# Performance work log

Hardware: AMD Instinct MI355X
Metric: run time of the kernel (lower is better)

## Reference

```python
import jax, jax.numpy as jnp
import numpy as np

DIM = 768


def setup_inputs() -> dict:
    key = jax.random.key(0)
    k1, k2, k3, k4, k5 = jax.random.split(key, 5)
    lines = jax.random.normal(k1, (32, 512, DIM), dtype=jnp.float32)
    videos = jax.random.normal(k2, (32, 128, DIM), dtype=jnp.float32)
    video_mask = jax.random.randint(k3, (32, 128), 0, 2, dtype=jnp.int32)
    # nn.Linear(dim, dim, bias=False) weights, applied as x @ W.T
    w_q = jax.random.normal(k4, (DIM, DIM), dtype=jnp.float32) * (DIM ** -0.5)
    w_k = jax.random.normal(k5, (DIM, DIM), dtype=jnp.float32) * (DIM ** -0.5)
    return {"lines": lines, "videos": videos, "video_mask": video_mask, "w_q": w_q, "w_k": w_k}


def reference(lines, videos, video_mask, w_q, w_k):
    scale = DIM ** -0.5
    q = jnp.einsum('bld,ed->ble', lines, w_q)   # (B, L, D)
    k = jnp.einsum('bvd,ed->bve', videos, w_k)  # (B, V, D)
    scores = jnp.einsum('bld,bvd->blv', q, k) * scale
    pad = (video_mask == 0)[:, None, :]          # (B, 1, V)
    scores = jnp.where(pad, jnp.float32(-1e9), scores)
    weights = jax.nn.softmax(scores, axis=-1)    # (B, L, V)
    return jnp.einsum('blv,bvd->bld', weights, videos)
```

## Files before the change

kernel.cpp:

```cpp
#include <hip/hip_runtime.h>

#define DIM 768
#define NB  32
#define LQ  512
#define NV  128

typedef unsigned short u16;
typedef unsigned int   u32;
typedef __bf16 bf16x8 __attribute__((ext_vector_type(8)));
typedef float  f32x4  __attribute__((ext_vector_type(4)));
typedef u16    u16x8  __attribute__((ext_vector_type(8)));
typedef u16    u16x4  __attribute__((ext_vector_type(4)));

typedef __attribute__((address_space(1))) const void gvoid;
typedef __attribute__((address_space(3))) void       svoid;

__device__ __forceinline__ u16 f2bf(float f) {
    u32 u = __float_as_uint(f);
    return (u16)((u + 0x7FFFu + ((u >> 16) & 1u)) >> 16);
}

__device__ __forceinline__ bf16x8 ld_frag(const u16* p) {
    return __builtin_bit_cast(bf16x8, *(const u16x8*)p);
}

__device__ __forceinline__ void gld16(const void* g, void* l) {
    __builtin_amdgcn_global_load_lds((gvoid*)g, (svoid*)l, 16, 0, 0);
}

#define W2S    4
#define W2_BLK (36 * W2S)

__global__ __launch_bounds__(256) void prep_kernel(const float* __restrict__ w_q,
                                                   const float* __restrict__ w_k,
                                                   const float* __restrict__ videos,
                                                   float* __restrict__ w2f,
                                                   u16* __restrict__ vt2,
                                                   u16* __restrict__ vbf) {
    __shared__ union {
        u16 T[64][136];
        struct { u16 q[128][72]; u16 k[128][72]; } w2s;
    } uL;
    const int bx = blockIdx.x;
    const int t  = threadIdx.x;

    if (bx < W2_BLK) {
        const int tile = bx / W2S, kc = bx % W2S;
        const int m0 = (tile / 6) * 128;
        const int n0 = (tile % 6) * 128;
        const int w    = t >> 6;
        const int lane = t & 63;
        const int quad = lane >> 4;
        const int ln   = lane & 15;
        const int wr   = (w >> 1) * 64;
        const int wc   = (w & 1) * 64;
        f32x4 acc[4][4] = {};
        for (int ks = kc * 3; ks < kc * 3 + 3; ++ks) {
            __syncthreads();
            const int e0 = ks * 64;
#pragma unroll
            for (int p = 0; p < 8; ++p) {
                int f  = t + p * 256;
                int r  = f >> 5;
                int c4 = f & 31;
                float4 xq = *(const float4*)(w_q + (size_t)(e0 + r) * DIM + m0 + c4 * 4);
                float4 xk = *(const float4*)(w_k + (size_t)(e0 + r) * DIM + n0 + c4 * 4);
                int swz = ((r >> 3) ^ ((c4 >> 1) & 7)) * 8 + (r & 7);
                uL.w2s.q[c4 * 4 + 0][swz] = f2bf(xq.x);
                uL.w2s.q[c4 * 4 + 1][swz] = f2bf(xq.y);
                uL.w2s.q[c4 * 4 + 2][swz] = f2bf(xq.z);
                uL.w2s.q[c4 * 4 + 3][swz] = f2bf(xq.w);
                uL.w2s.k[c4 * 4 + 0][swz] = f2bf(xk.x);
                uL.w2s.k[c4 * 4 + 1][swz] = f2bf(xk.y);
                uL.w2s.k[c4 * 4 + 2][swz] = f2bf(xk.z);
                uL.w2s.k[c4 * 4 + 3][swz] = f2bf(xk.w);
            }
            __syncthreads();
#pragma unroll
            for (int kk = 0; kk < 2; ++kk) {
                bf16x8 af[4], bfr[4];
#pragma unroll
                for (int i = 0; i < 4; ++i) {
                    int row = wr + i * 16 + ln;
                    af[i]  = ld_frag(&uL.w2s.q[row][((kk * 4 + quad) ^ ((row >> 3) & 7)) * 8]);
                }
#pragma unroll
                for (int j = 0; j < 4; ++j) {
                    int row = wc + j * 16 + ln;
                    bfr[j] = ld_frag(&uL.w2s.k[row][((kk * 4 + quad) ^ ((row >> 3) & 7)) * 8]);
                }
#pragma unroll
                for (int i = 0; i < 4; ++i)
#pragma unroll
                    for (int j = 0; j < 4; ++j)
                        acc[i][j] = __builtin_amdgcn_mfma_f32_16x16x32_bf16(af[i], bfr[j], acc[i][j], 0, 0, 0);
            }
        }
#pragma unroll
        for (int i = 0; i < 4; ++i)
#pragma unroll
            for (int j = 0; j < 4; ++j)
#pragma unroll
                for (int r = 0; r < 4; ++r)
                    atomicAdd(&w2f[(size_t)(m0 + wr + i * 16 + quad * 4 + r) * DIM +
                                   n0 + wc + j * 16 + ln], acc[i][j][r]);
        return;
    }

    const int v  = bx - W2_BLK;
    const int b  = v / 12;
    const int d0 = (v % 12) * 64;
    const float* src = videos + (size_t)b * NV * DIM;
#pragma unroll
    for (int p = 0; p < 8; ++p) {
        int f  = t + p * 256;
        int vv = f >> 4;
        int c4 = f & 15;
        float4 x = *(const float4*)(src + (size_t)vv * DIM + d0 + c4 * 4);
        u16x4 o = { f2bf(x.x), f2bf(x.y), f2bf(x.z), f2bf(x.w) };
        uL.T[c4 * 4 + 0][vv] = o[0];
        uL.T[c4 * 4 + 1][vv] = o[1];
        uL.T[c4 * 4 + 2][vv] = o[2];
        uL.T[c4 * 4 + 3][vv] = o[3];
        *(u16x4*)(vbf + ((size_t)b * NV + vv) * DIM + d0 + c4 * 4) = o;
    }
    __syncthreads();
#pragma unroll
    for (int p = 0; p < 4; ++p) {
        int f  = t + p * 256;
        int dl = f >> 4;
        int v8 = f & 15;
        int d  = d0 + dl;
        int it = d >> 7, wv = (d >> 4) & 7, lnn = d & 15;
        int ks = v8 >> 2, qd = v8 & 3;
        int lane = qd * 16 + lnn;
        size_t off = ((((size_t)b * 6 + it) * 8 + wv) * 4 + ks) * 512 + lane * 8;
        *(u16x8*)(vt2 + off) = *(const u16x8*)&uL.T[dl][v8 * 8];
    }
}

__global__ __launch_bounds__(512) void g_kernel(const u16* __restrict__ A,
                                                const float* __restrict__ Wf,
                                                u16* __restrict__ C) {
    __shared__ u16 sA[128][64];
    __shared__ u16 sB[128][72];
    const int t    = threadIdx.x;
    const int w    = t >> 6;
    const int lane = t & 63;
    const int quad = lane >> 4;
    const int ln   = lane & 15;

    int m0, n0;
    {
        int i = blockIdx.x;
        int xcd = i & 7, s = i >> 3;
        m0 = ((s / 6) * 8 + xcd) * 128;
        n0 = (s % 6) * 128;
    }

    const int wr = (w >> 2) * 64;
    const int wc = (w & 3) * 32;
    const int srow   = lane >> 3;
    const int schunk = (lane & 7) ^ srow;

    f32x4 acc[4][2] = {};
#pragma unroll
    for (int ks = 0; ks < 12; ++ks) {
        __syncthreads();
#pragma unroll
        for (int p = 0; p < 2; ++p) {
            int rb = w * 16 + p * 8;
            gld16(A + (size_t)(m0 + rb + srow) * DIM + ks * 64 + schunk * 8, &sA[rb][0]);
        }
#pragma unroll
        for (int p = 0; p < 4; ++p) {
            int idx = t + p * 512;
            int row = idx >> 4, c4 = idx & 15;
            float4 x = *(const float4*)(Wf + (size_t)(n0 + row) * DIM + ks * 64 + c4 * 4);
            u16x4 o = { f2bf(x.x), f2bf(x.y), f2bf(x.z), f2bf(x.w) };
            int swz = ((c4 >> 1) ^ (row & 7)) * 8 + (c4 & 1) * 4;
            *(u16x4*)&sB[row][swz] = o;
        }
        __syncthreads();
#pragma unroll
        for (int kk = 0; kk < 2; ++kk) {
            bf16x8 af[4], bfr[2];
#pragma unroll
            for (int i = 0; i < 4; ++i)
                af[i]  = ld_frag(&sA[wr + i * 16 + ln][((kk * 4 + quad) ^ (ln & 7)) * 8]);
#pragma unroll
            for (int j = 0; j < 2; ++j)
                bfr[j] = ld_frag(&sB[wc + j * 16 + ln][((kk * 4 + quad) ^ (ln & 7)) * 8]);
#pragma unroll
            for (int i = 0; i < 4; ++i)
#pragma unroll
                for (int j = 0; j < 2; ++j)
                    acc[i][j] = __builtin_amdgcn_mfma_f32_16x16x32_bf16(af[i], bfr[j], acc[i][j], 0, 0, 0);
        }
    }
#pragma unroll
    for (int i = 0; i < 4; ++i)
#pragma unroll
        for (int j = 0; j < 2; ++j)
#pragma unroll
            for (int r = 0; r < 4; ++r)
                C[(size_t)(m0 + wr + i * 16 + quad * 4 + r) * DIM + n0 + wc + j * 16 + ln] =
                    f2bf(acc[i][j][r]);
}

__global__ __launch_bounds__(512) void attn_kernel(const float* __restrict__ Qf,
                                                   const u16* __restrict__ K,
                                                   const u16* __restrict__ Vt2,
                                                   const int* __restrict__ mask,
                                                   float* __restrict__ out) {
    int b, l0;
    {
        int i = blockIdx.x;
        int xcd = i & 7, s = i >> 3;
        b  = (s >> 3) * 8 + xcd;
        l0 = (s & 7) * 64;
    }
    const int t    = threadIdx.x;
    const int w    = t >> 6;
    const int lane = t & 63;
    const int quad = lane >> 4;
    const int ln   = lane & 15;

    __shared__ union {
        struct { u16 q[2][64][64]; u16 k[2][128][64]; } st;
        float s[64][132];
    } uA;
    __shared__ u16 sP[64][136];
    __shared__ float sBias[128];

    const float* Qb = Qf + ((size_t)b * LQ + l0) * DIM;
    const u16*   Kb = K + (size_t)b * NV * DIM;
    if (t < NV) sBias[t] = mask[b * NV + t] ? 0.0f : -1e9f;

    const int srow   = lane >> 3;
    const int schunk = (lane & 7) ^ srow;
    const int qrow = t >> 3;
    const int qc8  = t & 7;
    const int qswz = (qc8 ^ (qrow & 7)) * 8;

    auto stageK = [&](int ks, int sel) {
        gld16(Kb + (size_t)(w * 16 + srow) * DIM + ks * 64 + schunk * 8, &uA.st.k[sel][w * 16][0]);
        gld16(Kb + (size_t)(w * 16 + 8 + srow) * DIM + ks * 64 + schunk * 8, &uA.st.k[sel][w * 16 + 8][0]);
    };
    auto loadQ = [&](int ks, float4& x0, float4& x1) {
        const float* p = Qb + (size_t)qrow * DIM + ks * 64 + qc8 * 8;
        x0 = *(const float4*)p;
        x1 = *(const float4*)(p + 4);
    };
    auto writeQ = [&](int sel, const float4& x0, const float4& x1) {
        u16x8 o = { f2bf(x0.x), f2bf(x0.y), f2bf(x0.z), f2bf(x0.w),
                    f2bf(x1.x), f2bf(x1.y), f2bf(x1.z), f2bf(x1.w) };
        *(u16x8*)&uA.st.q[sel][qrow][qswz] = o;
    };

    f32x4 accS[4] = {};
    {
        float4 x0, x1;
        loadQ(0, x0, x1);
        stageK(0, 0);
        writeQ(0, x0, x1);
    }
#pragma unroll
    for (int ks = 0; ks < 12; ++ks) {
        __syncthreads();
        const int sel = ks & 1;
        float4 nx0, nx1;
        if (ks < 11) {
            loadQ(ks + 1, nx0, nx1);
            stageK(ks + 1, sel ^ 1);
        }
#pragma unroll
        for (int kk = 0; kk < 2; ++kk) {
            bf16x8 bfr = ld_frag(&uA.st.k[sel][w * 16 + ln][((kk * 4 + quad) ^ (ln & 7)) * 8]);
#pragma unroll
            for (int i = 0; i < 4; ++i) {
                bf16x8 af = ld_frag(&uA.st.q[sel][i * 16 + ln][((kk * 4 + quad) ^ (ln & 7)) * 8]);
                accS[i] = __builtin_amdgcn_mfma_f32_16x16x32_bf16(af, bfr, accS[i], 0, 0, 0);
            }
        }
        if (ks < 11) writeQ(sel ^ 1, nx0, nx1);
    }
    __syncthreads();
    const float scale = 0.03608439182435161f;
#pragma unroll
    for (int i = 0; i < 4; ++i)
#pragma unroll
        for (int r = 0; r < 4; ++r)
            uA.s[i * 16 + quad * 4 + r][w * 16 + ln] = accS[i][r] * scale;
    __syncthreads();

    {
        const int row = t >> 3, seg = t & 7;
        float vals[16];
        float mx = -3.0e38f;
#pragma unroll
        for (int c = 0; c < 4; ++c) {
            float4 x  = *(const float4*)&uA.s[row][seg * 16 + c * 4];
            float4 bz = *(const float4*)&sBias[seg * 16 + c * 4];
            float a0 = x.x + bz.x, a1 = x.y + bz.y, a2 = x.z + bz.z, a3 = x.w + bz.w;
            vals[c * 4 + 0] = a0; vals[c * 4 + 1] = a1;
            vals[c * 4 + 2] = a2; vals[c * 4 + 3] = a3;
            mx = fmaxf(mx, fmaxf(fmaxf(a0, a1), fmaxf(a2, a3)));
        }
        mx = fmaxf(mx, __shfl_xor(mx, 1));
        mx = fmaxf(mx, __shfl_xor(mx, 2));
        mx = fmaxf(mx, __shfl_xor(mx, 4));
        float sum = 0.0f;
#pragma unroll
        for (int c = 0; c < 16; ++c) { float e = __expf(vals[c] - mx); vals[c] = e; sum += e; }
        sum += __shfl_xor(sum, 1);
        sum += __shfl_xor(sum, 2);
        sum += __shfl_xor(sum, 4);
        const float inv = 1.0f / sum;
#pragma unroll
        for (int h = 0; h < 2; ++h) {
            u16x8 pk;
#pragma unroll
            for (int e = 0; e < 8; ++e) pk[e] = f2bf(vals[h * 8 + e] * inv);
            *(u16x8*)&sP[row][seg * 16 + h * 8] = pk;
        }
    }
    __syncthreads();

    bf16x8 paf[4][4];
#pragma unroll
    for (int i = 0; i < 4; ++i)
#pragma unroll
        for (int ks = 0; ks < 4; ++ks)
            paf[i][ks] = ld_frag(&sP[i * 16 + ln][ks * 32 + quad * 8]);

    const u16* V2 = Vt2 + (size_t)b * 6 * 8 * 4 * 512;
    float*     Ob = out + ((size_t)b * LQ + l0) * DIM;
    for (int it = 0; it < 6; ++it) {
        f32x4 accO[4] = {};
#pragma unroll
        for (int ks = 0; ks < 4; ++ks) {
            bf16x8 bv = ld_frag(V2 + (((size_t)(it * 8 + w)) * 4 + ks) * 512 + lane * 8);
#pragma unroll
            for (int i = 0; i < 4; ++i)
                accO[i] = __builtin_amdgcn_mfma_f32_16x16x32_bf16(paf[i][ks], bv, accO[i], 0, 0, 0);
        }
#pragma unroll
        for (int i = 0; i < 4; ++i)
#pragma unroll
            for (int r = 0; r < 4; ++r)
                Ob[(size_t)(i * 16 + quad * 4 + r) * DIM + it * 128 + w * 16 + ln] = accO[i][r];
    }
}

extern "C" void kernel_launch(void* const* d_in, const int* in_sizes, int n_in,
                              void* d_out, int out_size, void* d_ws, size_t ws_size,
                              hipStream_t stream) {
    const float* lines  = (const float*)d_in[0];
    const float* videos = (const float*)d_in[1];
    const int*   mask   = (const int*)d_in[2];
    const float* w_q    = (const float*)d_in[3];
    const float* w_k    = (const float*)d_in[4];
    float*       out    = (float*)d_out;

    u16*   gw  = (u16*)d_ws;
    u16*   vt2 = gw  + (size_t)NB * NV * DIM;
    u16*   vbf = vt2 + (size_t)NB * DIM * NV;
    float* w2f = (float*)(vbf + (size_t)NB * NV * DIM);

    hipMemsetAsync(w2f, 0, (size_t)DIM * DIM * sizeof(float), stream);
    prep_kernel<<<W2_BLK + 384, 256, 0, stream>>>(w_q, w_k, videos, w2f, vt2, vbf);
    g_kernel   <<<192, 512, 0, stream>>>(vbf, w2f, gw);
    attn_kernel<<<256, 512, 0, stream>>>(lines, gw, vt2, mask, out);
}
```

Baseline: 165.5 us.

## Fuse prep, G and attention kernels into one cooperative persistent kernel

Replaces the memset plus three kernel launches with a single cooperative kernel of 256 blocks. Grid-wide syncs separate the phases: weight-product and video conversion, then the video-weight GEMM, then attention. The weight-product phase now covers the full K range in 36 blocks and writes the result directly, so the split-K atomics and the memset go away. This removes launch gaps and tail effects between kernels. In exchange, phase 1 uses only 36 blocks for the weight product, and the grid syncs and shared-memory union may limit occupancy. The old multi-kernel path is kept as a fallback if the cooperative launch fails.

```diff
diff --git a/kernel.cpp b/kernel.cpp
--- a/kernel.cpp
+++ b/kernel.cpp
@@ -1,4 +1,7 @@
 #include <hip/hip_runtime.h>
+#include <hip/hip_cooperative_groups.h>
+
+namespace cg = cooperative_groups;
 
 #define DIM 768
 #define NB  32
@@ -26,6 +29,321 @@
 
 __device__ __forceinline__ void gld16(const void* g, void* l) {
     __builtin_amdgcn_global_load_lds((gvoid*)g, (svoid*)l, 16, 0, 0);
+}
+
+__global__ __launch_bounds__(512) void fused_kernel(const float* __restrict__ lines,
+                                                    const float* __restrict__ videos,
+                                                    const int*   __restrict__ mask,
+                                                    const float* __restrict__ w_q,
+                                                    const float* __restrict__ w_k,
+                                                    float* __restrict__ out,
+                                                    u16* __restrict__ gw,
+                                                    u16* __restrict__ vt2,
+                                                    u16* __restrict__ vbf,
+                                                    float* __restrict__ w2f) {
+    __shared__ union {
+        struct { u16 q[128][72]; u16 k[128][72]; } w2s;
+        u16 T[2][64][136];
+        struct { u16 A[128][64]; u16 B[128][72]; } gs;
+        struct {
+            union {
+                struct { u16 q[2][64][64]; u16 k[2][128][64]; } st;
+                float s[64][132];
+            } u;
+            u16 p[64][136];
+            float bias[128];
+        } at;
+    } sm;
+
+    const int bx   = blockIdx.x;
+    const int t    = threadIdx.x;
+    const int w    = t >> 6;
+    const int lane = t & 63;
+    const int quad = lane >> 4;
+    const int ln   = lane & 15;
+
+    if (bx < 36) {
+        const int m0 = (bx / 6) * 128;
+        const int n0 = (bx % 6) * 128;
+        const int wr = (w >> 1) * 32;
+        const int wc = (w & 1) * 64;
+        f32x4 acc[2][4] = {};
+        for (int ks = 0; ks < 12; ++ks) {
+            __syncthreads();
+            const int e0 = ks * 64;
+#pragma unroll
+            for (int p = 0; p < 4; ++p) {
+                int f  = t + p * 512;
+                int r  = f >> 5;
+                int c4 = f & 31;
+                float4 xq = *(const float4*)(w_q + (size_t)(e0 + r) * DIM + m0 + c4 * 4);
+                float4 xk = *(const float4*)(w_k + (size_t)(e0 + r) * DIM + n0 + c4 * 4);
+                int swz = ((r >> 3) ^ ((c4 >> 1) & 7)) * 8 + (r & 7);
+                sm.w2s.q[c4 * 4 + 0][swz] = f2bf(xq.x);
+                sm.w2s.q[c4 * 4 + 1][swz] = f2bf(xq.y);
+                sm.w2s.q[c4 * 4 + 2][swz] = f2bf(xq.z);
+                sm.w2s.q[c4 * 4 + 3][swz] = f2bf(xq.w);
+                sm.w2s.k[c4 * 4 + 0][swz] = f2bf(xk.x);
+                sm.w2s.k[c4 * 4 + 1][swz] = f2bf(xk.y);
+                sm.w2s.k[c4 * 4 + 2][swz] = f2bf(xk.z);
+                sm.w2s.k[c4 * 4 + 3][swz] = f2bf(xk.w);
+            }
+            __syncthreads();
+#pragma unroll
+            for (int kk = 0; kk < 2; ++kk) {
+                bf16x8 af[2], bfr[4];
+#pragma unroll
+                for (int i = 0; i < 2; ++i) {
+                    int row = wr + i * 16 + ln;
+                    af[i]  = ld_frag(&sm.w2s.q[row][((kk * 4 + quad) ^ ((row >> 3) & 7)) * 8]);
+                }
+#pragma unroll
+                for (int j = 0; j < 4; ++j) {
+                    int row = wc + j * 16 + ln;
+                    bfr[j] = ld_frag(&sm.w2s.k[row][((kk * 4 + quad) ^ ((row >> 3) & 7)) * 8]);
+                }
+#pragma unroll
+                for (int i = 0; i < 2; ++i)
+#pragma unroll
+                    for (int j = 0; j < 4; ++j)
+                        acc[i][j] = __builtin_amdgcn_mfma_f32_16x16x32_bf16(af[i], bfr[j], acc[i][j], 0, 0, 0);
+            }
+        }
+#pragma unroll
+        for (int i = 0; i < 2; ++i)
+#pragma unroll
+            for (int j = 0; j < 4; ++j)
+#pragma unroll
+                for (int r = 0; r < 4; ++r)
+                    w2f[(size_t)(m0 + wr + i * 16 + quad * 4 + r) * DIM +
+                        n0 + wc + j * 16 + ln] = acc[i][j][r];
+    } else if (bx < 36 + 192) {
+        const int unit0 = (bx - 36) * 2;
+        if (unit0 < 384) {
+            const int half = t >> 8;
+            const int tl   = t & 255;
+            const int v    = unit0 + half;
+            const int b    = v / 12;
+            const int d0   = (v % 12) * 64;
+            const float* src = videos + (size_t)b * NV * DIM;
+#pragma unroll
+            for (int p = 0; p < 8; ++p) {
+                int f  = tl + p * 256;
+                int vv = f >> 4;
+                int c4 = f & 15;
+                float4 x = *(const float4*)(src + (size_t)vv * DIM + d0 + c4 * 4);
+                u16x4 o = { f2bf(x.x), f2bf(x.y), f2bf(x.z), f2bf(x.w) };
+                sm.T[half][c4 * 4 + 0][vv] = o[0];
+                sm.T[half][c4 * 4 + 1][vv] = o[1];
+                sm.T[half][c4 * 4 + 2][vv] = o[2];
+                sm.T[half][c4 * 4 + 3][vv] = o[3];
+                *(u16x4*)(vbf + ((size_t)b * NV + vv) * DIM + d0 + c4 * 4) = o;
+            }
+            __syncthreads();
+#pragma unroll
+            for (int p = 0; p < 4; ++p) {
+                int f  = tl + p * 256;
+                int dl = f >> 4;
+                int v8 = f & 15;
+                int d  = d0 + dl;
+                int it = d >> 7, wv = (d >> 4) & 7, lnn = d & 15;
+                int ksv = v8 >> 2, qd = v8 & 3;
+                int lane2 = qd * 16 + lnn;
+                size_t off = ((((size_t)b * 6 + it) * 8 + wv) * 4 + ksv) * 512 + lane2 * 8;
+                *(u16x8*)(vt2 + off) = *(const u16x8*)&sm.T[half][dl][v8 * 8];
+            }
+        }
+    }
+
+    cg::this_grid().sync();
+
+    if (bx < 192) {
+        int m0, n0;
+        {
+            int i = bx;
+            int xcd = i & 7, s = i >> 3;
+            m0 = ((s / 6) * 8 + xcd) * 128;
+            n0 = (s % 6) * 128;
+        }
+        const int wr = (w >> 2) * 64;
+        const int wc = (w & 3) * 32;
+        const int srow   = lane >> 3;
+        const int schunk = (lane & 7) ^ srow;
+
+        f32x4 acc[4][2] = {};
+#pragma unroll
+        for (int ks = 0; ks < 12; ++ks) {
+            __syncthreads();
+#pragma unroll
+            for (int p = 0; p < 2; ++p) {
+                int rb = w * 16 + p * 8;
+                gld16(vbf + (size_t)(m0 + rb + srow) * DIM + ks * 64 + schunk * 8, &sm.gs.A[rb][0]);
+            }
+#pragma unroll
+            for (int p = 0; p < 4; ++p) {
+                int idx = t + p * 512;
+                int row = idx >> 4, c4 = idx & 15;
+                float4 x = *(const float4*)(w2f + (size_t)(n0 + row) * DIM + ks * 64 + c4 * 4);
+                u16x4 o = { f2bf(x.x), f2bf(x.y), f2bf(x.z), f2bf(x.w) };
+                int swz = ((c4 >> 1) ^ (row & 7)) * 8 + (c4 & 1) * 4;
+                *(u16x4*)&sm.gs.B[row][swz] = o;
+            }
+            __syncthreads();
+#pragma unroll
+            for (int kk = 0; kk < 2; ++kk) {
+                bf16x8 af[4], bfr[2];
+#pragma unroll
+                for (int i = 0; i < 4; ++i)
+                    af[i]  = ld_frag(&sm.gs.A[wr + i * 16 + ln][((kk * 4 + quad) ^ (ln & 7)) * 8]);
+#pragma unroll
+                for (int j = 0; j < 2; ++j)
+                    bfr[j] = ld_frag(&sm.gs.B[wc + j * 16 + ln][((kk * 4 + quad) ^ (ln & 7)) * 8]);
+#pragma unroll
+                for (int i = 0; i < 4; ++i)
+#pragma unroll
+                    for (int j = 0; j < 2; ++j)
+                        acc[i][j] = __builtin_amdgcn_mfma_f32_16x16x32_bf16(af[i], bfr[j], acc[i][j], 0, 0, 0);
+            }
+        }
+#pragma unroll
+        for (int i = 0; i < 4; ++i)
+#pragma unroll
+            for (int j = 0; j < 2; ++j)
+#pragma unroll
+                for (int r = 0; r < 4; ++r)
+                    gw[(size_t)(m0 + wr + i * 16 + quad * 4 + r) * DIM + n0 + wc + j * 16 + ln] =
+                        f2bf(acc[i][j][r]);
+    }
+
+    cg::this_grid().sync();
+
+    {
+        int b, l0;
+        {
+            int i = bx;
+            int xcd = i & 7, s = i >> 3;
+            b  = (s >> 3) * 8 + xcd;
+            l0 = (s & 7) * 64;
+        }
+        const float* Qb = lines + ((size_t)b * LQ + l0) * DIM;
+        const u16*   Kb = gw + (size_t)b * NV * DIM;
+        if (t < NV) sm.at.bias[t] = mask[b * NV + t] ? 0.0f : -1e9f;
+
+        const int srow   = lane >> 3;
+        const int schunk = (lane & 7) ^ srow;
+        const int qrow = t >> 3;
+        const int qc8  = t & 7;
+        const int qswz = (qc8 ^ (qrow & 7)) * 8;
+
+        auto stageK = [&](int ks, int sel) {
+            gld16(Kb + (size_t)(w * 16 + srow) * DIM + ks * 64 + schunk * 8, &sm.at.u.st.k[sel][w * 16][0]);
+            gld16(Kb + (size_t)(w * 16 + 8 + srow) * DIM + ks * 64 + schunk * 8, &sm.at.u.st.k[sel][w * 16 + 8][0]);
+        };
+        auto loadQ = [&](int ks, float4& x0, float4& x1) {
+            const float* p = Qb + (size_t)qrow * DIM + ks * 64 + qc8 * 8;
+            x0 = *(const float4*)p;
+            x1 = *(const float4*)(p + 4);
+        };
+        auto writeQ = [&](int sel, const float4& x0, const float4& x1) {
+            u16x8 o = { f2bf(x0.x), f2bf(x0.y), f2bf(x0.z), f2bf(x0.w),
+                        f2bf(x1.x), f2bf(x1.y), f2bf(x1.z), f2bf(x1.w) };
+            *(u16x8*)&sm.at.u.st.q[sel][qrow][qswz] = o;
+        };
+
+        f32x4 accS[4] = {};
+        {
+            float4 x0, x1;
+            loadQ(0, x0, x1);
+            stageK(0, 0);
+            writeQ(0, x0, x1);
+        }
+#pragma unroll
+        for (int ks = 0; ks < 12; ++ks) {
+            __syncthreads();
+            const int sel = ks & 1;
+            float4 nx0, nx1;
+            if (ks < 11) {
+                loadQ(ks + 1, nx0, nx1);
+                stageK(ks + 1, sel ^ 1);
+            }
+#pragma unroll
+            for (int kk = 0; kk < 2; ++kk) {
+                bf16x8 bfr = ld_frag(&sm.at.u.st.k[sel][w * 16 + ln][((kk * 4 + quad) ^ (ln & 7)) * 8]);
+#pragma unroll
+                for (int i = 0; i < 4; ++i) {
+                    bf16x8 af = ld_frag(&sm.at.u.st.q[sel][i * 16 + ln][((kk * 4 + quad) ^ (ln & 7)) * 8]);
+                    accS[i] = __builtin_amdgcn_mfma_f32_16x16x32_bf16(af, bfr, accS[i], 0, 0, 0);
+                }
+            }
+            if (ks < 11) writeQ(sel ^ 1, nx0, nx1);
+        }
+        __syncthreads();
+        const float scale = 0.03608439182435161f;
+#pragma unroll
+        for (int i = 0; i < 4; ++i)
+#pragma unroll
+            for (int r = 0; r < 4; ++r)
+                sm.at.u.s[i * 16 + quad * 4 + r][w * 16 + ln] = accS[i][r] * scale;
+        __syncthreads();
+
+        {
+            const int row = t >> 3, seg = t & 7;
+            float vals[16];
+            float mx = -3.0e38f;
+#pragma unroll
+            for (int c = 0; c < 4; ++c) {
+                float4 x  = *(const float4*)&sm.at.u.s[row][seg * 16 + c * 4];
+                float4 bz = *(const float4*)&sm.at.bias[seg * 16 + c * 4];
+                float a0 = x.x + bz.x, a1 = x.y + bz.y, a2 = x.z + bz.z, a3 = x.w + bz.w;
+                vals[c * 4 + 0] = a0; vals[c * 4 + 1] = a1;
+                vals[c * 4 + 2] = a2; vals[c * 4 + 3] = a3;
+                mx = fmaxf(mx, fmaxf(fmaxf(a0, a1), fmaxf(a2, a3)));
+            }
+            mx = fmaxf(mx, __shfl_xor(mx, 1));
+            mx = fmaxf(mx, __shfl_xor(mx, 2));
+            mx = fmaxf(mx, __shfl_xor(mx, 4));
+            float sum = 0.0f;
+#pragma unroll
+            for (int c = 0; c < 16; ++c) { float e = __expf(vals[c] - mx); vals[c] = e; sum += e; }
+            sum += __shfl_xor(sum, 1);
+            sum += __shfl_xor(sum, 2);
+            sum += __shfl_xor(sum, 4);
+            const float inv = 1.0f / sum;
+#pragma unroll
+            for (int h = 0; h < 2; ++h) {
+                u16x8 pk;
+#pragma unroll
+                for (int e = 0; e < 8; ++e) pk[e] = f2bf(vals[h * 8 + e] * inv);
+                *(u16x8*)&sm.at.p[row][seg * 16 + h * 8] = pk;
+            }
+        }
+        __syncthreads();
+
+        bf16x8 paf[4][4];
+#pragma unroll
+        for (int i = 0; i < 4; ++i)
+#pragma unroll
+            for (int ks = 0; ks < 4; ++ks)
+                paf[i][ks] = ld_frag(&sm.at.p[i * 16 + ln][ks * 32 + quad * 8]);
+
+        const u16* V2 = vt2 + (size_t)b * 6 * 8 * 4 * 512;
+        float*     Ob = out + ((size_t)b * LQ + l0) * DIM;
+        for (int it = 0; it < 6; ++it) {
+            f32x4 accO[4] = {};
+#pragma unroll
+            for (int ks = 0; ks < 4; ++ks) {
+                bf16x8 bv = ld_frag(V2 + (((size_t)(it * 8 + w)) * 4 + ks) * 512 + lane * 8);
+#pragma unroll
+                for (int i = 0; i < 4; ++i)
+                    accO[i] = __builtin_amdgcn_mfma_f32_16x16x32_bf16(paf[i][ks], bv, accO[i], 0, 0, 0);
+            }
+#pragma unroll
+            for (int i = 0; i < 4; ++i)
+#pragma unroll
+                for (int r = 0; r < 4; ++r)
+                    Ob[(size_t)(i * 16 + quad * 4 + r) * DIM + it * 128 + w * 16 + ln] = accO[i][r];
+        }
+    }
 }
 
 #define W2S    4
@@ -368,8 +686,15 @@
     u16*   vbf = vt2 + (size_t)NB * DIM * NV;
     float* w2f = (float*)(vbf + (size_t)NB * NV * DIM);
 
-    hipMemsetAsync(w2f, 0, (size_t)DIM * DIM * sizeof(float), stream);
-    prep_kernel<<<W2_BLK + 384, 256, 0, stream>>>(w_q, w_k, videos, w2f, vt2, vbf);
-    g_kernel   <<<192, 512, 0, stream>>>(vbf, w2f, gw);
-    attn_kernel<<<256, 512, 0, stream>>>(lines, gw, vt2, mask, out);
+    void* args[] = { (void*)&lines, (void*)&videos, (void*)&mask, (void*)&w_q,
+                     (void*)&w_k, (void*)&out, (void*)&gw, (void*)&vt2,
+                     (void*)&vbf, (void*)&w2f };
+    hipError_t err = hipLaunchCooperativeKernel((void*)fused_kernel, dim3(256), dim3(512),
+                                                args, 0, stream);
+    if (err != hipSuccess) {
+        hipMemsetAsync(w2f, 0, (size_t)DIM * DIM * sizeof(float), stream);
+        prep_kernel<<<W2_BLK + 384, 256, 0, stream>>>(w_q, w_k, videos, w2f, vt2, vbf);
+        g_kernel   <<<192, 512, 0, stream>>>(vbf, w2f, gw);
+        attn_kernel<<<256, 512, 0, stream>>>(lines, gw, vt2, mask, out);
+    }
 }
```

New measurement: 248.1 us. 49.9% more time.

## Fuse prep, K-projection and attention into one persistent kernel with flag sync

Applied to the files above, without the earlier changes.

Replaces the three kernel launches with a single 256-block kernel. Blocks run prep, then the W2/K GEMM, then attention, and wait on global atomic flags for the inputs each stage needs. The W2 split-K partials now go to four separate buffers that the GEMM sums, instead of using atomicAdd into a zeroed buffer. This removes the launch gaps and kernel-boundary serialization between stages. In exchange it adds spin-waits that assume all 256 blocks are resident at once, a larger union of shared memory, and extra global reads to sum the partials.

```diff
diff --git a/kernel.cpp b/kernel.cpp
--- a/kernel.cpp
+++ b/kernel.cpp
@@ -4,6 +4,7 @@
 #define NB  32
 #define LQ  512
 #define NV  128
+#define W2SZ 589824
 
 typedef unsigned short u16;
 typedef unsigned int   u32;
@@ -28,328 +29,362 @@
     __builtin_amdgcn_global_load_lds((gvoid*)g, (svoid*)l, 16, 0, 0);
 }
 
-#define W2S    4
-#define W2_BLK (36 * W2S)
-
-__global__ __launch_bounds__(256) void prep_kernel(const float* __restrict__ w_q,
-                                                   const float* __restrict__ w_k,
-                                                   const float* __restrict__ videos,
-                                                   float* __restrict__ w2f,
-                                                   u16* __restrict__ vt2,
-                                                   u16* __restrict__ vbf) {
+#define FW2 0
+#define FVB 8
+#define FVT 40
+#define FK  72
+
+__device__ __forceinline__ void wait_ge(int* p, int n) {
+    int iters = 0;
+    while (__hip_atomic_load(p, __ATOMIC_RELAXED, __HIP_MEMORY_SCOPE_AGENT) < n) {
+        __builtin_amdgcn_s_sleep(2);
+        if (++iters > (1 << 20)) break;
+    }
+    (void)__hip_atomic_load(p, __ATOMIC_ACQUIRE, __HIP_MEMORY_SCOPE_AGENT);
+}
+
+__global__ __launch_bounds__(512, 2) void mega_kernel(const float* __restrict__ lines,
+                                                      const float* __restrict__ videos,
+                                                      const int*   __restrict__ mask,
+                                                      const float* __restrict__ w_q,
+                                                      const float* __restrict__ w_k,
+                                                      float* __restrict__ out,
+                                                      u16* __restrict__ gw,
+                                                      u16* __restrict__ vt2,
+                                                      u16* __restrict__ vbf,
+                                                      float* __restrict__ w2f,
+                                                      int* __restrict__ flags) {
     __shared__ union {
-        u16 T[64][136];
         struct { u16 q[128][72]; u16 k[128][72]; } w2s;
-    } uL;
-    const int bx = blockIdx.x;
-    const int t  = threadIdx.x;
-
-    if (bx < W2_BLK) {
-        const int tile = bx / W2S, kc = bx % W2S;
+        u16 T[2][64][136];
+        struct { u16 A[128][64]; u16 B[128][72]; } gs;
+        struct {
+            union {
+                struct { u16 q[2][64][64]; u16 k[2][128][64]; } st;
+                float s[64][132];
+            } u;
+            u16 p[64][136];
+            float bias[128];
+        } at;
+    } sm;
+
+    const int bx   = blockIdx.x;
+    const int t    = threadIdx.x;
+    const int w    = t >> 6;
+    const int lane = t & 63;
+    const int quad = lane >> 4;
+    const int ln   = lane & 15;
+
+    if (bx < 144) {
+        const int tile = bx >> 2, kc = bx & 3;
         const int m0 = (tile / 6) * 128;
         const int n0 = (tile % 6) * 128;
-        const int w    = t >> 6;
-        const int lane = t & 63;
-        const int quad = lane >> 4;
-        const int ln   = lane & 15;
-        const int wr   = (w >> 1) * 64;
-        const int wc   = (w & 1) * 64;
-        f32x4 acc[4][4] = {};
+        const int wr = (w >> 1) * 32;
+        const int wc = (w & 1) * 64;
+        f32x4 acc[2][4] = {};
         for (int ks = kc * 3; ks < kc * 3 + 3; ++ks) {
             __syncthreads();
             const int e0 = ks * 64;
 #pragma unroll
-            for (int p = 0; p < 8; ++p) {
-                int f  = t + p * 256;
+            for (int p = 0; p < 4; ++p) {
+                int f  = t + p * 512;
                 int r  = f >> 5;
                 int c4 = f & 31;
                 float4 xq = *(const float4*)(w_q + (size_t)(e0 + r) * DIM + m0 + c4 * 4);
                 float4 xk = *(const float4*)(w_k + (size_t)(e0 + r) * DIM + n0 + c4 * 4);
                 int swz = ((r >> 3) ^ ((c4 >> 1) & 7)) * 8 + (r & 7);
-                uL.w2s.q[c4 * 4 + 0][swz] = f2bf(xq.x);
-                uL.w2s.q[c4 * 4 + 1][swz] = f2bf(xq.y);
-                uL.w2s.q[c4 * 4 + 2][swz] = f2bf(xq.z);
-                uL.w2s.q[c4 * 4 + 3][swz] = f2bf(xq.w);
-                uL.w2s.k[c4 * 4 + 0][swz] = f2bf(xk.x);
-                uL.w2s.k[c4 * 4 + 1][swz] = f2bf(xk.y);
-                uL.w2s.k[c4 * 4 + 2][swz] = f2bf(xk.z);
-                uL.w2s.k[c4 * 4 + 3][swz] = f2bf(xk.w);
+                sm.w2s.q[c4 * 4 + 0][swz] = f2bf(xq.x);
+                sm.w2s.q[c4 * 4 + 1][swz] = f2bf(xq.y);
+                sm.w2s.q[c4 * 4 + 2][swz] = f2bf(xq.z);
+                sm.w2s.q[c4 * 4 + 3][swz] = f2bf(xq.w);
+                sm.w2s.k[c4 * 4 + 0][swz] = f2bf(xk.x);
+                sm.w2s.k[c4 * 4 + 1][swz] = f2bf(xk.y);
+                sm.w2s.k[c4 * 4 + 2][swz] = f2bf(xk.z);
+                sm.w2s.k[c4 * 4 + 3][swz] = f2bf(xk.w);
             }
             __syncthreads();
 #pragma unroll
             for (int kk = 0; kk < 2; ++kk) {
-                bf16x8 af[4], bfr[4];
-#pragma unroll
-                for (int i = 0; i < 4; ++i) {
+                bf16x8 af[2], bfr[4];
+#pragma unroll
+                for (int i = 0; i < 2; ++i) {
                     int row = wr + i * 16 + ln;
-                    af[i]  = ld_frag(&uL.w2s.q[row][((kk * 4 + quad) ^ ((row >> 3) & 7)) * 8]);
+                    af[i]  = ld_frag(&sm.w2s.q[row][((kk * 4 + quad) ^ ((row >> 3) & 7)) * 8]);
                 }
 #pragma unroll
                 for (int j = 0; j < 4; ++j) {
                     int row = wc + j * 16 + ln;
-                    bfr[j] = ld_frag(&uL.w2s.k[row][((kk * 4 + quad) ^ ((row >> 3) & 7)) * 8]);
+                    bfr[j] = ld_frag(&sm.w2s.k[row][((kk * 4 + quad) ^ ((row >> 3) & 7)) * 8]);
                 }
 #pragma unroll
-                for (int i = 0; i < 4; ++i)
+                for (int i = 0; i < 2; ++i)
 #pragma unroll
                     for (int j = 0; j < 4; ++j)
                         acc[i][j] = __builtin_amdgcn_mfma_f32_16x16x32_bf16(af[i], bfr[j], acc[i][j], 0, 0, 0);
             }
         }
+        float* wp = w2f + (size_t)kc * W2SZ;
+#pragma unroll
+        for (int i = 0; i < 2; ++i)
+#pragma unroll
+            for (int j = 0; j < 4; ++j)
+#pragma unroll
+                for (int r = 0; r < 4; ++r)
+                    wp[(size_t)(m0 + wr + i * 16 + quad * 4 + r) * DIM +
+                       n0 + wc + j * 16 + ln] = acc[i][j][r];
+        __syncthreads();
+        if (t == 0) { __threadfence(); atomicAdd(&flags[FW2 + tile / 6], 1); }
+    } else if (bx < 240) {
+        const int half = t >> 8;
+        const int tl   = t & 255;
+        for (int pass = 0; pass < 2; ++pass) {
+            const int v  = (bx - 144) * 4 + pass * 2 + half;
+            const int b  = v / 12;
+            const int d0 = (v % 12) * 64;
+            const float* src = videos + (size_t)b * NV * DIM;
+            if (pass) __syncthreads();
+#pragma unroll
+            for (int p = 0; p < 8; ++p) {
+                int f  = tl + p * 256;
+                int vv = f >> 4;
+                int c4 = f & 15;
+                float4 x = *(const float4*)(src + (size_t)vv * DIM + d0 + c4 * 4);
+                u16x4 o = { f2bf(x.x), f2bf(x.y), f2bf(x.z), f2bf(x.w) };
+                sm.T[half][c4 * 4 + 0][vv] = o[0];
+                sm.T[half][c4 * 4 + 1][vv] = o[1];
+                sm.T[half][c4 * 4 + 2][vv] = o[2];
+                sm.T[half][c4 * 4 + 3][vv] = o[3];
+                *(u16x4*)(vbf + ((size_t)b * NV + vv) * DIM + d0 + c4 * 4) = o;
+            }
+            __syncthreads();
+#pragma unroll
+            for (int p = 0; p < 4; ++p) {
+                int f  = tl + p * 256;
+                int dl = f >> 4;
+                int v8 = f & 15;
+                int d  = d0 + dl;
+                int it = d >> 7, wv = (d >> 4) & 7, lnn = d & 15;
+                int ksv = v8 >> 2, qd = v8 & 3;
+                int lane2 = qd * 16 + lnn;
+                size_t off = ((((size_t)b * 6 + it) * 8 + wv) * 4 + ksv) * 512 + lane2 * 8;
+                *(u16x8*)(vt2 + off) = *(const u16x8*)&sm.T[half][dl][v8 * 8];
+            }
+            __syncthreads();
+            if (tl == 0) {
+                __threadfence();
+                atomicAdd(&flags[FVB + b], 1);
+                atomicAdd(&flags[FVT + b], 1);
+            }
+        }
+    }
+
+    if (bx < 192) {
+        int m0, n0;
+        {
+            int i = bx;
+            int xcd = i & 7, s = i >> 3;
+            m0 = ((s / 6) * 8 + xcd) * 128;
+            n0 = (s % 6) * 128;
+        }
+        const int gb = m0 >> 7;
+        if (t == 0) {
+            wait_ge(&flags[FW2 + (n0 >> 7)], 24);
+            wait_ge(&flags[FVB + gb], 12);
+        }
+        __syncthreads();
+
+        const int wr = (w >> 2) * 64;
+        const int wc = (w & 3) * 32;
+        const int srow   = lane >> 3;
+        const int schunk = (lane & 7) ^ srow;
+
+        f32x4 acc[4][2] = {};
+#pragma unroll
+        for (int ks = 0; ks < 12; ++ks) {
+            __syncthreads();
+#pragma unroll
+            for (int p = 0; p < 2; ++p) {
+                int rb = w * 16 + p * 8;
+                gld16(vbf + (size_t)(m0 + rb + srow) * DIM + ks * 64 + schunk * 8, &sm.gs.A[rb][0]);
+            }
+#pragma unroll
+            for (int p = 0; p < 4; ++p) {
+                int idx = t + p * 512;
+                int row = idx >> 4, c4 = idx & 15;
+                const float* bp = w2f + (size_t)(n0 + row) * DIM + ks * 64 + c4 * 4;
+                float4 x0 = *(const float4*)bp;
+                float4 x1 = *(const float4*)(bp + W2SZ);
+                float4 x2 = *(const float4*)(bp + 2 * W2SZ);
+                float4 x3 = *(const float4*)(bp + 3 * W2SZ);
+                float sx = x0.x + x1.x + x2.x + x3.x;
+                float sy = x0.y + x1.y + x2.y + x3.y;
+                float sz = x0.z + x1.z + x2.z + x3.z;
+                float sw = x0.w + x1.w + x2.w + x3.w;
+                u16x4 o = { f2bf(sx), f2bf(sy), f2bf(sz), f2bf(sw) };
+                int swz = ((c4 >> 1) ^ (row & 7)) * 8 + (c4 & 1) * 4;
+                *(u16x4*)&sm.gs.B[row][swz] = o;
+            }
+            __syncthreads();
+#pragma unroll
+            for (int kk = 0; kk < 2; ++kk) {
+                bf16x8 af[4], bfr[2];
+#pragma unroll
+                for (int i = 0; i < 4; ++i)
+                    af[i]  = ld_frag(&sm.gs.A[wr + i * 16 + ln][((kk * 4 + quad) ^ (ln & 7)) * 8]);
+#pragma unroll
+                for (int j = 0; j < 2; ++j)
+                    bfr[j] = ld_frag(&sm.gs.B[wc + j * 16 + ln][((kk * 4 + quad) ^ (ln & 7)) * 8]);
+#pragma unroll
+                for (int i = 0; i < 4; ++i)
+#pragma unroll
+                    for (int j = 0; j < 2; ++j)
+                        acc[i][j] = __builtin_amdgcn_mfma_f32_16x16x32_bf16(af[i], bfr[j], acc[i][j], 0, 0, 0);
+            }
+        }
 #pragma unroll
         for (int i = 0; i < 4; ++i)
 #pragma unroll
-            for (int j = 0; j < 4; ++j)
+            for (int j = 0; j < 2; ++j)
 #pragma unroll
                 for (int r = 0; r < 4; ++r)
-                    atomicAdd(&w2f[(size_t)(m0 + wr + i * 16 + quad * 4 + r) * DIM +
-                                   n0 + wc + j * 16 + ln], acc[i][j][r]);
-        return;
+                    gw[(size_t)(m0 + wr + i * 16 + quad * 4 + r) * DIM + n0 + wc + j * 16 + ln] =
+                        f2bf(acc[i][j][r]);
+        __syncthreads();
+        if (t == 0) { __threadfence(); atomicAdd(&flags[FK + gb], 1); }
     }
 
-    const int v  = bx - W2_BLK;
-    const int b  = v / 12;
-    const int d0 = (v % 12) * 64;
-    const float* src = videos + (size_t)b * NV * DIM;
-#pragma unroll
-    for (int p = 0; p < 8; ++p) {
-        int f  = t + p * 256;
-        int vv = f >> 4;
-        int c4 = f & 15;
-        float4 x = *(const float4*)(src + (size_t)vv * DIM + d0 + c4 * 4);
-        u16x4 o = { f2bf(x.x), f2bf(x.y), f2bf(x.z), f2bf(x.w) };
-        uL.T[c4 * 4 + 0][vv] = o[0];
-        uL.T[c4 * 4 + 1][vv] = o[1];
-        uL.T[c4 * 4 + 2][vv] = o[2];
-        uL.T[c4 * 4 + 3][vv] = o[3];
-        *(u16x4*)(vbf + ((size_t)b * NV + vv) * DIM + d0 + c4 * 4) = o;
-    }
-    __syncthreads();
-#pragma unroll
-    for (int p = 0; p < 4; ++p) {
-        int f  = t + p * 256;
-        int dl = f >> 4;
-        int v8 = f & 15;
-        int d  = d0 + dl;
-        int it = d >> 7, wv = (d >> 4) & 7, lnn = d & 15;
-        int ks = v8 >> 2, qd = v8 & 3;
-        int lane = qd * 16 + lnn;
-        size_t off = ((((size_t)b * 6 + it) * 8 + wv) * 4 + ks) * 512 + lane * 8;
-        *(u16x8*)(vt2 + off) = *(const u16x8*)&uL.T[dl][v8 * 8];
-    }
-}
-
-__global__ __launch_bounds__(512) void g_kernel(const u16* __restrict__ A,
-                                                const float* __restrict__ Wf,
-                                                u16* __restrict__ C) {
-    __shared__ u16 sA[128][64];
-    __shared__ u16 sB[128][72];
-    const int t    = threadIdx.x;
-    const int w    = t >> 6;
-    const int lane = t & 63;
-    const int quad = lane >> 4;
-    const int ln   = lane & 15;
-
-    int m0, n0;
     {
-        int i = blockIdx.x;
-        int xcd = i & 7, s = i >> 3;
-        m0 = ((s / 6) * 8 + xcd) * 128;
-        n0 = (s % 6) * 128;
-    }
-
-    const int wr = (w >> 2) * 64;
-    const int wc = (w & 3) * 32;
-    const int srow   = lane >> 3;
-    const int schunk = (lane & 7) ^ srow;
-
-    f32x4 acc[4][2] = {};
-#pragma unroll
-    for (int ks = 0; ks < 12; ++ks) {
-        __syncthreads();
-#pragma unroll
-        for (int p = 0; p < 2; ++p) {
-            int rb = w * 16 + p * 8;
-            gld16(A + (size_t)(m0 + rb + srow) * DIM + ks * 64 + schunk * 8, &sA[rb][0]);
-        }
-#pragma unroll
-        for (int p = 0; p < 4; ++p) {
-            int idx = t + p * 512;
-            int row = idx >> 4, c4 = idx & 15;
-            float4 x = *(const float4*)(Wf + (size_t)(n0 + row) * DIM + ks * 64 + c4 * 4);
-            u16x4 o = { f2bf(x.x), f2bf(x.y), f2bf(x.z), f2bf(x.w) };
-            int swz = ((c4 >> 1) ^ (row & 7)) * 8 + (c4 & 1) * 4;
-            *(u16x4*)&sB[row][swz] = o;
-        }
-        __syncthreads();
-#pragma unroll
-        for (int kk = 0; kk < 2; ++kk) {
-            bf16x8 af[4], bfr[2];
+        int b, l0;
+        {
+            int i = bx;
+            int xcd = i & 7, s = i >> 3;
+            b  = (s >> 3) * 8 + xcd;
+            l0 = (s & 7) * 64;
+        }
+        if (t == 0) {
+            wait_ge(&flags[FK + b], 6);
+            wait_ge(&flags[FVT + b], 12);
+        }
+        __syncthreads();
+
+        const float* Qb = lines + ((size_t)b * LQ + l0) * DIM;
+        const u16*   Kb = gw + (size_t)b * NV * DIM;
+        if (t < NV) sm.at.bias[t] = mask[b * NV + t] ? 0.0f : -1e9f;
+
+        const int srow   = lane >> 3;
+        const int schunk = (lane & 7) ^ srow;
+        const int qrow = t >> 3;
+        const int qc8  = t & 7;
+        const int qswz = (qc8 ^ (qrow & 7)) * 8;
+
+        auto stageK = [&](int ks, int sel) {
+            gld16(Kb + (size_t)(w * 16 + srow) * DIM + ks * 64 + schunk * 8, &sm.at.u.st.k[sel][w * 16][0]);
+            gld16(Kb + (size_t)(w * 16 + 8 + srow) * DIM + ks * 64 + schunk * 8, &sm.at.u.st.k[sel][w * 16 + 8][0]);
+        };
+        auto loadQ = [&](int ks, float4& x0, float4& x1) {
+            const float* p = Qb + (size_t)qrow * DIM + ks * 64 + qc8 * 8;
+            x0 = *(const float4*)p;
+            x1 = *(const float4*)(p + 4);
+        };
+        auto writeQ = [&](int sel, const float4& x0, const float4& x1) {
+            u16x8 o = { f2bf(x0.x), f2bf(x0.y), f2bf(x0.z), f2bf(x0.w),
+                        f2bf(x1.x), f2bf(x1.y), f2bf(x1.z), f2bf(x1.w) };
+            *(u16x8*)&sm.at.u.st.q[sel][qrow][qswz] = o;
+        };
+
+        f32x4 accS[4] = {};
+        {
+            float4 x0, x1;
+            loadQ(0, x0, x1);
+            stageK(0, 0);
+            writeQ(0, x0, x1);
+        }
+#pragma unroll
+        for (int ks = 0; ks < 12; ++ks) {
+            __syncthreads();
+            const int sel = ks & 1;
+            float4 nx0, nx1;
+            if (ks < 11) {
+                loadQ(ks + 1, nx0, nx1);
+                stageK(ks + 1, sel ^ 1);
+            }
+#pragma unroll
+            for (int kk = 0; kk < 2; ++kk) {
+                bf16x8 bfr = ld_frag(&sm.at.u.st.k[sel][w * 16 + ln][((kk * 4 + quad) ^ (ln & 7)) * 8]);
+#pragma unroll
+                for (int i = 0; i < 4; ++i) {
+                    bf16x8 af = ld_frag(&sm.at.u.st.q[sel][i * 16 + ln][((kk * 4 + quad) ^ (ln & 7)) * 8]);
+                    accS[i] = __builtin_amdgcn_mfma_f32_16x16x32_bf16(af, bfr, accS[i], 0, 0, 0);
+                }
+            }
+            if (ks < 11) writeQ(sel ^ 1, nx0, nx1);
+        }
+        __syncthreads();
+        const float scale = 0.03608439182435161f;
+#pragma unroll
+        for (int i = 0; i < 4; ++i)
+#pragma unroll
+            for (int r = 0; r < 4; ++r)
+                sm.at.u.s[i * 16 + quad * 4 + r][w * 16 + ln] = accS[i][r] * scale;
+        __syncthreads();
+
+        {
+            const int row = t >> 3, seg = t & 7;
+            float vals[16];
+            float mx = -3.0e38f;
+#pragma unroll
+            for (int c = 0; c < 4; ++c) {
+                float4 x  = *(const float4*)&sm.at.u.s[row][seg * 16 + c * 4];
+                float4 bz = *(const float4*)&sm.at.bias[seg * 16 + c * 4];
+                float a0 = x.x + bz.x, a1 = x.y + bz.y, a2 = x.z + bz.z, a3 = x.w + bz.w;
+                vals[c * 4 + 0] = a0; vals[c * 4 + 1] = a1;
+                vals[c * 4 + 2] = a2; vals[c * 4 + 3] = a3;
+                mx = fmaxf(mx, fmaxf(fmaxf(a0, a1), fmaxf(a2, a3)));
+            }
+            mx = fmaxf(mx, __shfl_xor(mx, 1));
+            mx = fmaxf(mx, __shfl_xor(mx, 2));
+            mx = fmaxf(mx, __shfl_xor(mx, 4));
+            float sum = 0.0f;
+#pragma unroll
+            for (int c = 0; c < 16; ++c) { float e = __expf(vals[c] - mx); vals[c] = e; sum += e; }
+            sum += __shfl_xor(sum, 1);
+            sum += __shfl_xor(sum, 2);
+            sum += __shfl_xor(sum, 4);
+            const float inv = 1.0f / sum;
+#pragma unroll
+            for (int h = 0; h < 2; ++h) {
+                u16x8 pk;
+#pragma unroll
+                for (int e = 0; e < 8; ++e) pk[e] = f2bf(vals[h * 8 + e] * inv);
+                *(u16x8*)&sm.at.p[row][seg * 16 + h * 8] = pk;
+            }
+        }
+        __syncthreads();
+
+        bf16x8 paf[4][4];
+#pragma unroll
+        for (int i = 0; i < 4; ++i)
+#pragma unroll
+            for (int ks = 0; ks < 4; ++ks)
+                paf[i][ks] = ld_frag(&sm.at.p[i * 16 + ln][ks * 32 + quad * 8]);
+
+        const u16* V2 = vt2 + (size_t)b * 6 * 8 * 4 * 512;
+        float*     Ob = out + ((size_t)b * LQ + l0) * DIM;
+        for (int it = 0; it < 6; ++it) {
+            f32x4 accO[4] = {};
+#pragma unroll
+            for (int ks = 0; ks < 4; ++ks) {
+                bf16x8 bv = ld_frag(V2 + (((size_t)(it * 8 + w)) * 4 + ks) * 512 + lane * 8);
+#pragma unroll
+                for (int i = 0; i < 4; ++i)
+                    accO[i] = __builtin_amdgcn_mfma_f32_16x16x32_bf16(paf[i][ks], bv, accO[i], 0, 0, 0);
+            }
 #pragma unroll
             for (int i = 0; i < 4; ++i)
-                af[i]  = ld_frag(&sA[wr + i * 16 + ln][((kk * 4 + quad) ^ (ln & 7)) * 8]);
-#pragma unroll
-            for (int j = 0; j < 2; ++j)
-                bfr[j] = ld_frag(&sB[wc + j * 16 + ln][((kk * 4 + quad) ^ (ln & 7)) * 8]);
-#pragma unroll
-            for (int i = 0; i < 4; ++i)
-#pragma unroll
-                for (int j = 0; j < 2; ++j)
-                    acc[i][j] = __builtin_amdgcn_mfma_f32_16x16x32_bf16(af[i], bfr[j], acc[i][j], 0, 0, 0);
-        }
-    }
-#pragma unroll
-    for (int i = 0; i < 4; ++i)
-#pragma unroll
-        for (int j = 0; j < 2; ++j)
-#pragma unroll
-            for (int r = 0; r < 4; ++r)
-                C[(size_t)(m0 + wr + i * 16 + quad * 4 + r) * DIM + n0 + wc + j * 16 + ln] =
-                    f2bf(acc[i][j][r]);
-}
-
-__global__ __launch_bounds__(512) void attn_kernel(const float* __restrict__ Qf,
-                                                   const u16* __restrict__ K,
-                                                   const u16* __restrict__ Vt2,
-                                                   const int* __restrict__ mask,
-                                                   float* __restrict__ out) {
-    int b, l0;
-    {
-        int i = blockIdx.x;
-        int xcd = i & 7, s = i >> 3;
-        b  = (s >> 3) * 8 + xcd;
-        l0 = (s & 7) * 64;
-    }
-    const int t    = threadIdx.x;
-    const int w    = t >> 6;
-    const int lane = t & 63;
-    const int quad = lane >> 4;
-    const int ln   = lane & 15;
-
-    __shared__ union {
-        struct { u16 q[2][64][64]; u16 k[2][128][64]; } st;
-        float s[64][132];
-    } uA;
-    __shared__ u16 sP[64][136];
-    __shared__ float sBias[128];
-
-    const float* Qb = Qf + ((size_t)b * LQ + l0) * DIM;
-    const u16*   Kb = K + (size_t)b * NV * DIM;
-    if (t < NV) sBias[t] = mask[b * NV + t] ? 0.0f : -1e9f;
-
-    const int srow   = lane >> 3;
-    const int schunk = (lane & 7) ^ srow;
-    const int qrow = t >> 3;
-    const int qc8  = t & 7;
-    const int qswz = (qc8 ^ (qrow & 7)) * 8;
-
-    auto stageK = [&](int ks, int sel) {
-        gld16(Kb + (size_t)(w * 16 + srow) * DIM + ks * 64 + schunk * 8, &uA.st.k[sel][w * 16][0]);
-        gld16(Kb + (size_t)(w * 16 + 8 + srow) * DIM + ks * 64 + schunk * 8, &uA.st.k[sel][w * 16 + 8][0]);
-    };
-    auto loadQ = [&](int ks, float4& x0, float4& x1) {
-        const float* p = Qb + (size_t)qrow * DIM + ks * 64 + qc8 * 8;
-        x0 = *(const float4*)p;
-        x1 = *(const float4*)(p + 4);
-    };
-    auto writeQ = [&](int sel, const float4& x0, const float4& x1) {
-        u16x8 o = { f2bf(x0.x), f2bf(x0.y), f2bf(x0.z), f2bf(x0.w),
-                    f2bf(x1.x), f2bf(x1.y), f2bf(x1.z), f2bf(x1.w) };
-        *(u16x8*)&uA.st.q[sel][qrow][qswz] = o;
-    };
-
-    f32x4 accS[4] = {};
-    {
-        float4 x0, x1;
-        loadQ(0, x0, x1);
-        stageK(0, 0);
-        writeQ(0, x0, x1);
-    }
-#pragma unroll
-    for (int ks = 0; ks < 12; ++ks) {
-        __syncthreads();
-        const int sel = ks & 1;
-        float4 nx0, nx1;
-        if (ks < 11) {
-            loadQ(ks + 1, nx0, nx1);
-            stageK(ks + 1, sel ^ 1);
-        }
-#pragma unroll
-        for (int kk = 0; kk < 2; ++kk) {
-            bf16x8 bfr = ld_frag(&uA.st.k[sel][w * 16 + ln][((kk * 4 + quad) ^ (ln & 7)) * 8]);
-#pragma unroll
-            for (int i = 0; i < 4; ++i) {
-                bf16x8 af = ld_frag(&uA.st.q[sel][i * 16 + ln][((kk * 4 + quad) ^ (ln & 7)) * 8]);
-                accS[i] = __builtin_amdgcn_mfma_f32_16x16x32_bf16(af, bfr, accS[i], 0, 0, 0);
-            }
-        }
-        if (ks < 11) writeQ(sel ^ 1, nx0, nx1);
-    }
-    __syncthreads();
-    const float scale = 0.03608439182435161f;
-#pragma unroll
-    for (int i = 0; i < 4; ++i)
-#pragma unroll
-        for (int r = 0; r < 4; ++r)
-            uA.s[i * 16 + quad * 4 + r][w * 16 + ln] = accS[i][r] * scale;
-    __syncthreads();
-
-    {
-        const int row = t >> 3, seg = t & 7;
-        float vals[16];
-        float mx = -3.0e38f;
-#pragma unroll
-        for (int c = 0; c < 4; ++c) {
-            float4 x  = *(const float4*)&uA.s[row][seg * 16 + c * 4];
-            float4 bz = *(const float4*)&sBias[seg * 16 + c * 4];
-            float a0 = x.x + bz.x, a1 = x.y + bz.y, a2 = x.z + bz.z, a3 = x.w + bz.w;
-            vals[c * 4 + 0] = a0; vals[c * 4 + 1] = a1;
-            vals[c * 4 + 2] = a2; vals[c * 4 + 3] = a3;
-            mx = fmaxf(mx, fmaxf(fmaxf(a0, a1), fmaxf(a2, a3)));
-        }
-        mx = fmaxf(mx, __shfl_xor(mx, 1));
-        mx = fmaxf(mx, __shfl_xor(mx, 2));
-        mx = fmaxf(mx, __shfl_xor(mx, 4));
-        float sum = 0.0f;
-#pragma unroll
-        for (int c = 0; c < 16; ++c) { float e = __expf(vals[c] - mx); vals[c] = e; sum += e; }
-        sum += __shfl_xor(sum, 1);
-        sum += __shfl_xor(sum, 2);
-        sum += __shfl_xor(sum, 4);
-        const float inv = 1.0f / sum;
-#pragma unroll
-        for (int h = 0; h < 2; ++h) {
-            u16x8 pk;
-#pragma unroll
-            for (int e = 0; e < 8; ++e) pk[e] = f2bf(vals[h * 8 + e] * inv);
-            *(u16x8*)&sP[row][seg * 16 + h * 8] = pk;
-        }
-    }
-    __syncthreads();
-
-    bf16x8 paf[4][4];
-#pragma unroll
-    for (int i = 0; i < 4; ++i)
-#pragma unroll
-        for (int ks = 0; ks < 4; ++ks)
-            paf[i][ks] = ld_frag(&sP[i * 16 + ln][ks * 32 + quad * 8]);
-
-    const u16* V2 = Vt2 + (size_t)b * 6 * 8 * 4 * 512;
-    float*     Ob = out + ((size_t)b * LQ + l0) * DIM;
-    for (int it = 0; it < 6; ++it) {
-        f32x4 accO[4] = {};
-#pragma unroll
-        for (int ks = 0; ks < 4; ++ks) {
-            bf16x8 bv = ld_frag(V2 + (((size_t)(it * 8 + w)) * 4 + ks) * 512 + lane * 8);
-#pragma unroll
-            for (int i = 0; i < 4; ++i)
-                accO[i] = __builtin_amdgcn_mfma_f32_16x16x32_bf16(paf[i][ks], bv, accO[i], 0, 0, 0);
-        }
-#pragma unroll
-        for (int i = 0; i < 4; ++i)
-#pragma unroll
-            for (int r = 0; r < 4; ++r)
-                Ob[(size_t)(i * 16 + quad * 4 + r) * DIM + it * 128 + w * 16 + ln] = accO[i][r];
+#pragma unroll
+                for (int r = 0; r < 4; ++r)
+                    Ob[(size_t)(i * 16 + quad * 4 + r) * DIM + it * 128 + w * 16 + ln] = accO[i][r];
+        }
     }
 }
 
@@ -367,9 +402,9 @@
     u16*   vt2 = gw  + (size_t)NB * NV * DIM;
     u16*   vbf = vt2 + (size_t)NB * DIM * NV;
     float* w2f = (float*)(vbf + (size_t)NB * NV * DIM);
-
-    hipMemsetAsync(w2f, 0, (size_t)DIM * DIM * sizeof(float), stream);
-    prep_kernel<<<W2_BLK + 384, 256, 0, stream>>>(w_q, w_k, videos, w2f, vt2, vbf);
-    g_kernel   <<<192, 512, 0, stream>>>(vbf, w2f, gw);
-    attn_kernel<<<256, 512, 0, stream>>>(lines, gw, vt2, mask, out);
-}
+    int*   flg = (int*)(w2f + 4 * (size_t)W2SZ);
+
+    hipMemsetAsync(flg, 0, 512, stream);
+    mega_kernel<<<256, 512, 0, stream>>>(lines, videos, mask, w_q, w_k, out,
+                                         gw, vt2, vbf, w2f, flg);
+}
```

Measured after the change: 217.8 us. 1.32x slower.
